# Kernel tuning notes

Measured on AMD Instinct MI355X. Metric: run time of the kernel, lower is better.

The kernel has to match this reference:

```python
import jax, jax.numpy as jnp
import numpy as np

B, L, H, NH = 8, 384, 512, 8
DH = H // NH
MAX_SEQ_LEN = 384


def setup_inputs() -> dict:
    key = jax.random.key(0)
    ks = jax.random.split(key, 16)
    s = 0.02
    seq_len = jnp.concatenate([
        jnp.array([L], dtype=jnp.int32),
        jax.random.randint(ks[3], (B - 1,), L // 2, L + 1, dtype=jnp.int32),
    ])
    return {
        "key": jax.random.normal(ks[0], (B, L, H), jnp.float32),
        "query": jax.random.normal(ks[1], (B, L, H), jnp.float32),
        "value": jax.random.normal(ks[2], (B, L, H), jnp.float32),
        "seq_len": seq_len,
        "pe": jax.random.normal(ks[4], (2 * MAX_SEQ_LEN + 1, H), jnp.float32) * s,
        "Wk": jax.random.normal(ks[5], (H, H), jnp.float32) * s,
        "bk": jnp.zeros((H,), jnp.float32),
        "Wq": jax.random.normal(ks[6], (H, H), jnp.float32) * s,
        "bq": jnp.zeros((H,), jnp.float32),
        "Wv": jax.random.normal(ks[7], (H, H), jnp.float32) * s,
        "bv": jnp.zeros((H,), jnp.float32),
        "Wr": jax.random.normal(ks[8], (H, H), jnp.float32) * s,
        "br": jnp.zeros((H,), jnp.float32),
        "u_bias": jax.random.normal(ks[9], (NH, DH), jnp.float32) * s,
        "v_bias": jax.random.normal(ks[10], (NH, DH), jnp.float32) * s,
        "Wff": jax.random.normal(ks[11], (H, H), jnp.float32) * s,
        "bff": jnp.zeros((H,), jnp.float32),
    }


def reference(key, query, value, seq_len, pe, Wk, bk, Wq, bq, Wv, bv, Wr, br, u_bias, v_bias, Wff, bff):
    # relative distances: rel[i, j] = j - i, in [-(L-1), L-1]
    rel = jnp.arange(L)[None, :] - jnp.arange(L)[:, None]          # [L, L]
    rpe = pe[rel + MAX_SEQ_LEN]                                    # [L, L, H]

    k = (key @ Wk.T + bk).reshape(B, L, NH, DH)
    q = (query @ Wq.T + bq).reshape(B, L, NH, DH)
    v = (value @ Wv.T + bv).reshape(B, L, NH, DH)
    rpe = (rpe @ Wr.T + br).reshape(L, L, NH, DH)

    # Transformer-XL score terms
    A = jnp.einsum('bihd,bjhd->bhij', q, k)                        # content-content
    Bt = jnp.einsum('bihd,ijhd->bhij', q, rpe)                     # content-position
    C = jnp.einsum('hd,bjhd->bhj', u_bias, k)[:, :, None, :]       # global content bias
    Dt = jnp.einsum('hd,ijhd->hij', v_bias, rpe)[None]             # global position bias

    scores = (A + Bt + C + Dt) / jnp.sqrt(jnp.float32(DH))
    key_mask = jnp.arange(L)[None, :] < seq_len[:, None]           # [B, L]
    scores = jnp.where(key_mask[:, None, None, :], scores, -1e15)
    attn = jax.nn.softmax(scores, axis=-1)                         # [B, NH, L, L]

    out = jnp.einsum('bhij,bjhd->bihd', attn, v).reshape(B, L, H)
    return out @ Wff.T + bff
```

## Files before the change

kernel.cpp:

```cpp
#include <hip/hip_runtime.h>
#include <hip/hip_bf16.h>

#define B_  8
#define L_  384
#define H_  512
#define NH_ 8
#define DH_ 64
#define RRM 768

typedef short bf16x8 __attribute__((ext_vector_type(8)));
typedef float f32x4  __attribute__((ext_vector_type(4)));
#define MFMA_BF16 __builtin_amdgcn_mfma_f32_16x16x32_bf16

static __device__ __forceinline__ unsigned short f2bf(float f) {
    unsigned u = __builtin_bit_cast(unsigned, f);
    u += 0x7fffu + ((u >> 16) & 1u);
    return (unsigned short)(u >> 16);
}
static __device__ __forceinline__ float bf2f(unsigned short s) {
    unsigned u = ((unsigned)s) << 16;
    return __builtin_bit_cast(float, u);
}

struct CvtArgs {
    const float* src[9];
    unsigned short* dst[9];
    int nchunks[9];
};
__global__ __launch_bounds__(256) void cvt_kernel(CvtArgs a) {
    int chunk = blockIdx.x;
    int r = 0;
    while (r < 8 && chunk >= a.nchunks[r]) { chunk -= a.nchunks[r]; r++; }
    const float4 v = ((const float4*)a.src[r])[chunk * 256 + threadIdx.x];
    ushort4 o;
    o.x = f2bf(v.x); o.y = f2bf(v.y); o.z = f2bf(v.z); o.w = f2bf(v.w);
    ((ushort4*)a.dst[r])[chunk * 256 + threadIdx.x] = o;
}

#define LDT 72

template <bool IS_FF>
__global__ __launch_bounds__(256) void gemm_nt(
    const unsigned short* __restrict__ A0, const unsigned short* __restrict__ A1,
    const unsigned short* __restrict__ A2, const unsigned short* __restrict__ A3,
    const unsigned short* __restrict__ W0, const unsigned short* __restrict__ W1,
    const unsigned short* __restrict__ W2, const unsigned short* __restrict__ W3,
    const float* __restrict__ b0, const float* __restrict__ b1,
    const float* __restrict__ b2, const float* __restrict__ b3,
    const float* __restrict__ ub, const float* __restrict__ vbias,
    unsigned short* __restrict__ qu, unsigned short* __restrict__ qv,
    unsigned short* __restrict__ kb, unsigned short* __restrict__ vT,
    unsigned short* __restrict__ rp, float* __restrict__ ff) {

    const int z = IS_FF ? 4 : blockIdx.z;
    if (!IS_FF && z == 3 && blockIdx.y >= 12) return;
    const unsigned short* A = IS_FF ? A0 : (z == 0 ? A0 : z == 1 ? A1 : z == 2 ? A2 : A3);
    const unsigned short* W = IS_FF ? W0 : (z == 0 ? W0 : z == 1 ? W1 : z == 2 ? W2 : W3);
    const float* bias       = IS_FF ? b0 : (z == 0 ? b0 : z == 1 ? b1 : z == 2 ? b2 : b3);

    __shared__ unsigned short As[2][64 * LDT];
    __shared__ unsigned short Bs[2][64 * LDT];

    const int tid = threadIdx.x;
    const int w = tid >> 6, lane = tid & 63;
    const int quad = lane >> 4, lm = lane & 15;
    const int l8r = lane >> 3, l8c = lane & 7;
    const int wr = (w & 1) * 32, wc = (w >> 1) * 32;

    const unsigned short* ag = A + (size_t)(blockIdx.y * 64 + w * 16 + l8r) * 512 + l8c * 8;
    const unsigned short* wg = W + (size_t)(blockIdx.x * 64 + w * 16 + l8r) * 512 + l8c * 8;
    const int soff = (w * 16 + l8r) * LDT + l8c * 8;

    bf16x8 pa0 = *(const bf16x8*)(ag);
    bf16x8 pa1 = *(const bf16x8*)(ag + 8 * 512);
    bf16x8 pb0 = *(const bf16x8*)(wg);
    bf16x8 pb1 = *(const bf16x8*)(wg + 8 * 512);
    *(bf16x8*)&As[0][soff]            = pa0;
    *(bf16x8*)&As[0][soff + 8 * LDT]  = pa1;
    *(bf16x8*)&Bs[0][soff]            = pb0;
    *(bf16x8*)&Bs[0][soff + 8 * LDT]  = pb1;

    f32x4 acc[2][2] = {};
    for (int kc = 0; kc < 8; ++kc) {
        __syncthreads();
        const int buf = kc & 1;
        if (kc < 7) {
            const int k0 = (kc + 1) * 64;
            pa0 = *(const bf16x8*)(ag + k0);
            pa1 = *(const bf16x8*)(ag + k0 + 8 * 512);
            pb0 = *(const bf16x8*)(wg + k0);
            pb1 = *(const bf16x8*)(wg + k0 + 8 * 512);
        }
        #pragma unroll
        for (int ks = 0; ks < 2; ++ks) {
            bf16x8 a0 = *(const bf16x8*)&As[buf][(wr + lm) * LDT + ks * 32 + quad * 8];
            bf16x8 a1 = *(const bf16x8*)&As[buf][(wr + 16 + lm) * LDT + ks * 32 + quad * 8];
            bf16x8 w0 = *(const bf16x8*)&Bs[buf][(wc + lm) * LDT + ks * 32 + quad * 8];
            bf16x8 w1 = *(const bf16x8*)&Bs[buf][(wc + 16 + lm) * LDT + ks * 32 + quad * 8];
            acc[0][0] = MFMA_BF16(a0, w0, acc[0][0], 0, 0, 0);
            acc[0][1] = MFMA_BF16(a0, w1, acc[0][1], 0, 0, 0);
            acc[1][0] = MFMA_BF16(a1, w0, acc[1][0], 0, 0, 0);
            acc[1][1] = MFMA_BF16(a1, w1, acc[1][1], 0, 0, 0);
        }
        if (kc < 7) {
            const int nb = buf ^ 1;
            *(bf16x8*)&As[nb][soff]           = pa0;
            *(bf16x8*)&As[nb][soff + 8 * LDT] = pa1;
            *(bf16x8*)&Bs[nb][soff]           = pb0;
            *(bf16x8*)&Bs[nb][soff + 8 * LDT] = pb1;
        }
    }

    #pragma unroll
    for (int si = 0; si < 2; ++si) {
        #pragma unroll
        for (int sj = 0; sj < 2; ++sj) {
            #pragma unroll
            for (int reg = 0; reg < 4; ++reg) {
                const int r = blockIdx.y * 64 + wr + si * 16 + quad * 4 + reg;
                const int c = blockIdx.x * 64 + wc + sj * 16 + lm;
                const float val = acc[si][sj][reg] + bias[c];
                if (IS_FF) {
                    ff[r * 512 + c] = val;
                } else if (z == 0) {
                    const int bb = r / L_, ii = r - bb * L_;
                    const int h = c >> 6, d = c & 63;
                    const int idx = ((bb * NH_ + h) * L_ + ii) * DH_ + d;
                    qu[idx] = f2bf((val + ub[c]) * 0.125f);
                    qv[idx] = f2bf((val + vbias[c]) * 0.125f);
                } else if (z == 1) {
                    const int bb = r / L_, ii = r - bb * L_;
                    const int h = c >> 6, d = c & 63;
                    kb[((bb * NH_ + h) * L_ + ii) * DH_ + d] = f2bf(val);
                } else if (z == 2) {
                    const int bb = r / L_, ii = r - bb * L_;
                    const int h = c >> 6, d = c & 63;
                    vT[((bb * NH_ + h) * DH_ + d) * L_ + ii] = f2bf(val);
                } else {
                    rp[r * 512 + c] = f2bf(val);
                }
            }
        }
    }
}

#define BTSTR 424
__global__ __launch_bounds__(256) void attn_fused(
    const unsigned short* __restrict__ qu, const unsigned short* __restrict__ qv,
    const unsigned short* __restrict__ kbf, const unsigned short* __restrict__ vT,
    const unsigned short* __restrict__ rp, const int* __restrict__ seq_len,
    unsigned short* __restrict__ Obf) {
    __shared__ __align__(16) unsigned short BtP[32 * BTSTR];
    __shared__ float mx_red[32][2];
    __shared__ float sm_red[32][2];
    const int lane = threadIdx.x & 63, wv = threadIdx.x >> 6;
    const int quad = lane >> 4, lm = lane & 15;
    const int bh = blockIdx.y, b = bh >> 3, h = bh & 7;
    const int i0 = blockIdx.x * 32;
    const int sl = seq_len[b];
    const int msub = wv & 1, nh = wv >> 1;
    const int m_lo = 353 - i0;
    const int i_fr = i0 + msub * 16 + lm;

    {
        const unsigned short* qvr = qv + (size_t)(bh * L_ + i_fr) * DH_;
        const bf16x8 av0 = *(const bf16x8*)(qvr + quad * 8);
        const bf16x8 av1 = *(const bf16x8*)(qvr + 32 + quad * 8);
        #pragma unroll
        for (int ns = 0; ns < 13; ++ns) {
            const int n = nh * 208 + ns * 16 + lm;
            const unsigned short* rrow = rp + (size_t)(m_lo + n) * 512 + h * 64;
            f32x4 bacc = {};
            bacc = MFMA_BF16(av0, *(const bf16x8*)(rrow + quad * 8), bacc, 0, 0, 0);
            bacc = MFMA_BF16(av1, *(const bf16x8*)(rrow + 32 + quad * 8), bacc, 0, 0, 0);
            #pragma unroll
            for (int reg = 0; reg < 4; ++reg) {
                const int il = msub * 16 + quad * 4 + reg;
                BtP[il * BTSTR + n] = f2bf(bacc[reg]);
            }
        }
    }
    const unsigned short* qur = qu + (size_t)(bh * L_ + i_fr) * DH_;
    const bf16x8 au0 = *(const bf16x8*)(qur + quad * 8);
    const bf16x8 au1 = *(const bf16x8*)(qur + 32 + quad * 8);
    __syncthreads();

    f32x4 sc[12];
    #pragma unroll
    for (int ns = 0; ns < 12; ++ns) {
        const int j = nh * 192 + ns * 16 + lm;
        const unsigned short* krow = kbf + (size_t)(bh * L_ + j) * DH_;
        f32x4 a = {};
        a = MFMA_BF16(au0, *(const bf16x8*)(krow + quad * 8), a, 0, 0, 0);
        a = MFMA_BF16(au1, *(const bf16x8*)(krow + 32 + quad * 8), a, 0, 0, 0);
        sc[ns] = a;
    }
    const int jbase = nh * 192 + lm;
    #pragma unroll
    for (int ns = 0; ns < 12; ++ns) {
        const int j = jbase + ns * 16;
        #pragma unroll
        for (int reg = 0; reg < 4; ++reg) {
            const int il = msub * 16 + quad * 4 + reg;
            float val = -1e30f;
            if (j < sl) val = sc[ns][reg] + bf2f(BtP[il * BTSTR + (j - il + 31)]);
            sc[ns][reg] = val;
        }
    }

    const int il0 = msub * 16 + quad * 4;
    float mx4[4], sm4[4], inv4[4];
    #pragma unroll
    for (int reg = 0; reg < 4; ++reg) {
        float m = sc[0][reg];
        #pragma unroll
        for (int ns = 1; ns < 12; ++ns) m = fmaxf(m, sc[ns][reg]);
        #pragma unroll
        for (int o = 1; o < 16; o <<= 1) m = fmaxf(m, __shfl_xor(m, o));
        mx4[reg] = m;
    }
    if (lm == 0) {
        #pragma unroll
        for (int reg = 0; reg < 4; ++reg) mx_red[il0 + reg][nh] = mx4[reg];
    }
    __syncthreads();
    #pragma unroll
    for (int reg = 0; reg < 4; ++reg)
        mx4[reg] = fmaxf(mx_red[il0 + reg][0], mx_red[il0 + reg][1]);
    #pragma unroll
    for (int reg = 0; reg < 4; ++reg) sm4[reg] = 0.f;
    #pragma unroll
    for (int ns = 0; ns < 12; ++ns) {
        #pragma unroll
        for (int reg = 0; reg < 4; ++reg) {
            const float e = __expf(sc[ns][reg] - mx4[reg]);
            sc[ns][reg] = e;
            sm4[reg] += e;
        }
    }
    #pragma unroll
    for (int reg = 0; reg < 4; ++reg) {
        float s = sm4[reg];
        #pragma unroll
        for (int o = 1; o < 16; o <<= 1) s += __shfl_xor(s, o);
        sm4[reg] = s;
    }
    if (lm == 0) {
        #pragma unroll
        for (int reg = 0; reg < 4; ++reg) sm_red[il0 + reg][nh] = sm4[reg];
    }
    __syncthreads();
    #pragma unroll
    for (int reg = 0; reg < 4; ++reg)
        inv4[reg] = 1.f / (sm_red[il0 + reg][0] + sm_red[il0 + reg][1]);

    #pragma unroll
    for (int ns = 0; ns < 12; ++ns) {
        const int j = jbase + ns * 16;
        #pragma unroll
        for (int reg = 0; reg < 4; ++reg)
            BtP[(il0 + reg) * BTSTR + j] = f2bf(sc[ns][reg] * inv4[reg]);
    }
    __syncthreads();

    {
        const int pr = msub * 16 + lm;
        f32x4 oacc[2] = {};
        #pragma unroll
        for (int kc = 0; kc < 12; ++kc) {
            const bf16x8 af = *(const bf16x8*)&BtP[pr * BTSTR + kc * 32 + quad * 8];
            #pragma unroll
            for (int t = 0; t < 2; ++t) {
                const int n = nh * 32 + t * 16 + lm;
                const unsigned short* vrow = vT + (size_t)(bh * DH_ + n) * L_ + kc * 32 + quad * 8;
                oacc[t] = MFMA_BF16(af, *(const bf16x8*)(vrow), oacc[t], 0, 0, 0);
            }
        }
        #pragma unroll
        for (int t = 0; t < 2; ++t) {
            #pragma unroll
            for (int reg = 0; reg < 4; ++reg) {
                const int i = i0 + msub * 16 + quad * 4 + reg;
                const int d = nh * 32 + t * 16 + lm;
                Obf[(size_t)(b * L_ + i) * H_ + h * DH_ + d] = f2bf(oacc[t][reg]);
            }
        }
    }
}

extern "C" void kernel_launch(void* const* d_in, const int* in_sizes, int n_in,
                              void* d_out, int out_size, void* d_ws, size_t ws_size,
                              hipStream_t stream) {
    const float* key    = (const float*)d_in[0];
    const float* query  = (const float*)d_in[1];
    const float* value  = (const float*)d_in[2];
    const int*   seqlen = (const int*)d_in[3];
    const float* pe     = (const float*)d_in[4];
    const float* Wk     = (const float*)d_in[5];
    const float* bk     = (const float*)d_in[6];
    const float* Wq     = (const float*)d_in[7];
    const float* bq     = (const float*)d_in[8];
    const float* Wv     = (const float*)d_in[9];
    const float* bv     = (const float*)d_in[10];
    const float* Wr     = (const float*)d_in[11];
    const float* br     = (const float*)d_in[12];
    const float* u_bias = (const float*)d_in[13];
    const float* v_bias = (const float*)d_in[14];
    const float* Wff    = (const float*)d_in[15];
    const float* bff    = (const float*)d_in[16];

    const size_t nTok  = (size_t)B_ * L_ * H_;
    const size_t nW    = (size_t)H_ * H_;
    const size_t nPe   = (size_t)RRM * H_;
    unsigned short* p  = (unsigned short*)d_ws;
    unsigned short* qbf  = p; p += nTok;
    unsigned short* kin  = p; p += nTok;
    unsigned short* vin  = p; p += nTok;
    unsigned short* pebf = p; p += nPe;
    unsigned short* Wqb  = p; p += nW;
    unsigned short* Wkb  = p; p += nW;
    unsigned short* Wvb  = p; p += nW;
    unsigned short* Wrb  = p; p += nW;
    unsigned short* Wffb = p; p += nW;
    unsigned short* qu   = p; p += nTok;
    unsigned short* qv   = p; p += nTok;
    unsigned short* kb   = p; p += nTok;
    unsigned short* vT   = p; p += nTok;
    unsigned short* rp   = p; p += nPe + 512;
    unsigned short* Obf  = qbf;

    CvtArgs ca;
    ca.src[0] = query;  ca.dst[0] = qbf;  ca.nchunks[0] = 1536;
    ca.src[1] = key;    ca.dst[1] = kin;  ca.nchunks[1] = 1536;
    ca.src[2] = value;  ca.dst[2] = vin;  ca.nchunks[2] = 1536;
    ca.src[3] = pe;     ca.dst[3] = pebf; ca.nchunks[3] = 384;
    ca.src[4] = Wq;     ca.dst[4] = Wqb;  ca.nchunks[4] = 256;
    ca.src[5] = Wk;     ca.dst[5] = Wkb;  ca.nchunks[5] = 256;
    ca.src[6] = Wv;     ca.dst[6] = Wvb;  ca.nchunks[6] = 256;
    ca.src[7] = Wr;     ca.dst[7] = Wrb;  ca.nchunks[7] = 256;
    ca.src[8] = Wff;    ca.dst[8] = Wffb; ca.nchunks[8] = 256;
    cvt_kernel<<<6272, 256, 0, stream>>>(ca);

    gemm_nt<false><<<dim3(8, 48, 4), 256, 0, stream>>>(
        qbf, kin, vin, pebf, Wqb, Wkb, Wvb, Wrb, bq, bk, bv, br,
        u_bias, v_bias, qu, qv, kb, vT, rp, nullptr);

    attn_fused<<<dim3(L_ / 32, B_ * NH_), 256, 0, stream>>>(
        qu, qv, kb, vT, rp, seqlen, Obf);

    gemm_nt<true><<<dim3(8, 48, 1), 256, 0, stream>>>(
        Obf, nullptr, nullptr, nullptr, Wffb, nullptr, nullptr, nullptr,
        bff, nullptr, nullptr, nullptr, nullptr, nullptr,
        nullptr, nullptr, nullptr, nullptr, nullptr, (float*)d_out);
}
```

Before: 161.9 us.

## Fuse fp32-to-bf16 conversion into GEMM loads and skip masked key tiles

Removes the standalone conversion kernel. The projection GEMMs now read fp32 activations and weights directly and convert them to bf16 while staging into shared memory, which saves a full read/write pass over the inputs and one kernel launch. The attention kernel also skips QK and position-score MFMA tiles, and the PV loop iterations, that lie beyond each batch's seq_len. The cost is that the GEMMs load twice the bytes per tile and convert redundantly, since weights are converted again in every block. The variable trip counts also add branch divergence.

```diff
diff --git a/kernel.cpp b/kernel.cpp
--- a/kernel.cpp
+++ b/kernel.cpp
@@ -21,32 +21,31 @@
     unsigned u = ((unsigned)s) << 16;
     return __builtin_bit_cast(float, u);
 }
-
-struct CvtArgs {
-    const float* src[9];
-    unsigned short* dst[9];
-    int nchunks[9];
-};
-__global__ __launch_bounds__(256) void cvt_kernel(CvtArgs a) {
-    int chunk = blockIdx.x;
-    int r = 0;
-    while (r < 8 && chunk >= a.nchunks[r]) { chunk -= a.nchunks[r]; r++; }
-    const float4 v = ((const float4*)a.src[r])[chunk * 256 + threadIdx.x];
-    ushort4 o;
-    o.x = f2bf(v.x); o.y = f2bf(v.y); o.z = f2bf(v.z); o.w = f2bf(v.w);
-    ((ushort4*)a.dst[r])[chunk * 256 + threadIdx.x] = o;
+static __device__ __forceinline__ unsigned pack2(float lo, float hi) {
+    return (unsigned)f2bf(lo) | ((unsigned)f2bf(hi) << 16);
+}
+static __device__ __forceinline__ void cvt_store8(unsigned short* dst, float4 a, float4 b) {
+    uint4 o;
+    o.x = pack2(a.x, a.y);
+    o.y = pack2(a.z, a.w);
+    o.z = pack2(b.x, b.y);
+    o.w = pack2(b.z, b.w);
+    *(uint4*)dst = o;
 }
 
 #define LDT 72
 
 template <bool IS_FF>
 __global__ __launch_bounds__(256) void gemm_nt(
-    const unsigned short* __restrict__ A0, const unsigned short* __restrict__ A1,
-    const unsigned short* __restrict__ A2, const unsigned short* __restrict__ A3,
-    const unsigned short* __restrict__ W0, const unsigned short* __restrict__ W1,
-    const unsigned short* __restrict__ W2, const unsigned short* __restrict__ W3,
+    const float* __restrict__ A0f, const float* __restrict__ A1f,
+    const float* __restrict__ A2f, const float* __restrict__ A3f,
+    const unsigned short* __restrict__ Abf,
+    const float* __restrict__ W0, const float* __restrict__ W1,
+    const float* __restrict__ W2, const float* __restrict__ W3,
+    const float* __restrict__ W4,
     const float* __restrict__ b0, const float* __restrict__ b1,
     const float* __restrict__ b2, const float* __restrict__ b3,
+    const float* __restrict__ b4,
     const float* __restrict__ ub, const float* __restrict__ vbias,
     unsigned short* __restrict__ qu, unsigned short* __restrict__ qv,
     unsigned short* __restrict__ kb, unsigned short* __restrict__ vT,
@@ -54,9 +53,9 @@
 
     const int z = IS_FF ? 4 : blockIdx.z;
     if (!IS_FF && z == 3 && blockIdx.y >= 12) return;
-    const unsigned short* A = IS_FF ? A0 : (z == 0 ? A0 : z == 1 ? A1 : z == 2 ? A2 : A3);
-    const unsigned short* W = IS_FF ? W0 : (z == 0 ? W0 : z == 1 ? W1 : z == 2 ? W2 : W3);
-    const float* bias       = IS_FF ? b0 : (z == 0 ? b0 : z == 1 ? b1 : z == 2 ? b2 : b3);
+    const float* Af   = IS_FF ? nullptr : (z == 0 ? A0f : z == 1 ? A1f : z == 2 ? A2f : A3f);
+    const float* W    = IS_FF ? W4 : (z == 0 ? W0 : z == 1 ? W1 : z == 2 ? W2 : W3);
+    const float* bias = IS_FF ? b4 : (z == 0 ? b0 : z == 1 ? b1 : z == 2 ? b2 : b3);
 
     __shared__ unsigned short As[2][64 * LDT];
     __shared__ unsigned short Bs[2][64 * LDT];
@@ -67,18 +66,32 @@
     const int l8r = lane >> 3, l8c = lane & 7;
     const int wr = (w & 1) * 32, wc = (w >> 1) * 32;
 
-    const unsigned short* ag = A + (size_t)(blockIdx.y * 64 + w * 16 + l8r) * 512 + l8c * 8;
-    const unsigned short* wg = W + (size_t)(blockIdx.x * 64 + w * 16 + l8r) * 512 + l8c * 8;
+    const size_t arow = (size_t)blockIdx.y * 64 + w * 16 + l8r;
+    const size_t wrow = (size_t)blockIdx.x * 64 + w * 16 + l8r;
+    const float* agf = IS_FF ? nullptr : Af + arow * 512 + l8c * 8;
+    const unsigned short* agb = IS_FF ? Abf + arow * 512 + l8c * 8 : nullptr;
+    const float* wgf = W + wrow * 512 + l8c * 8;
     const int soff = (w * 16 + l8r) * LDT + l8c * 8;
 
-    bf16x8 pa0 = *(const bf16x8*)(ag);
-    bf16x8 pa1 = *(const bf16x8*)(ag + 8 * 512);
-    bf16x8 pb0 = *(const bf16x8*)(wg);
-    bf16x8 pb1 = *(const bf16x8*)(wg + 8 * 512);
-    *(bf16x8*)&As[0][soff]            = pa0;
-    *(bf16x8*)&As[0][soff + 8 * LDT]  = pa1;
-    *(bf16x8*)&Bs[0][soff]            = pb0;
-    *(bf16x8*)&Bs[0][soff + 8 * LDT]  = pb1;
+    float4 pw0, pw1, pw2, pw3;
+    float4 pa0, pa1, pa2, pa3;
+    bf16x8 pab0, pab1;
+
+    pw0 = *(const float4*)(wgf);           pw1 = *(const float4*)(wgf + 4);
+    pw2 = *(const float4*)(wgf + 8 * 512); pw3 = *(const float4*)(wgf + 8 * 512 + 4);
+    if constexpr (!IS_FF) {
+        pa0 = *(const float4*)(agf);           pa1 = *(const float4*)(agf + 4);
+        pa2 = *(const float4*)(agf + 8 * 512); pa3 = *(const float4*)(agf + 8 * 512 + 4);
+        cvt_store8(&As[0][soff], pa0, pa1);
+        cvt_store8(&As[0][soff + 8 * LDT], pa2, pa3);
+    } else {
+        pab0 = *(const bf16x8*)(agb);
+        pab1 = *(const bf16x8*)(agb + 8 * 512);
+        *(bf16x8*)&As[0][soff] = pab0;
+        *(bf16x8*)&As[0][soff + 8 * LDT] = pab1;
+    }
+    cvt_store8(&Bs[0][soff], pw0, pw1);
+    cvt_store8(&Bs[0][soff + 8 * LDT], pw2, pw3);
 
     f32x4 acc[2][2] = {};
     for (int kc = 0; kc < 8; ++kc) {
@@ -86,10 +99,15 @@
         const int buf = kc & 1;
         if (kc < 7) {
             const int k0 = (kc + 1) * 64;
-            pa0 = *(const bf16x8*)(ag + k0);
-            pa1 = *(const bf16x8*)(ag + k0 + 8 * 512);
-            pb0 = *(const bf16x8*)(wg + k0);
-            pb1 = *(const bf16x8*)(wg + k0 + 8 * 512);
+            pw0 = *(const float4*)(wgf + k0);           pw1 = *(const float4*)(wgf + k0 + 4);
+            pw2 = *(const float4*)(wgf + k0 + 8 * 512); pw3 = *(const float4*)(wgf + k0 + 8 * 512 + 4);
+            if constexpr (!IS_FF) {
+                pa0 = *(const float4*)(agf + k0);           pa1 = *(const float4*)(agf + k0 + 4);
+                pa2 = *(const float4*)(agf + k0 + 8 * 512); pa3 = *(const float4*)(agf + k0 + 8 * 512 + 4);
+            } else {
+                pab0 = *(const bf16x8*)(agb + k0);
+                pab1 = *(const bf16x8*)(agb + k0 + 8 * 512);
+            }
         }
         #pragma unroll
         for (int ks = 0; ks < 2; ++ks) {
@@ -104,10 +122,15 @@
         }
         if (kc < 7) {
             const int nb = buf ^ 1;
-            *(bf16x8*)&As[nb][soff]           = pa0;
-            *(bf16x8*)&As[nb][soff + 8 * LDT] = pa1;
-            *(bf16x8*)&Bs[nb][soff]           = pb0;
-            *(bf16x8*)&Bs[nb][soff + 8 * LDT] = pb1;
+            if constexpr (!IS_FF) {
+                cvt_store8(&As[nb][soff], pa0, pa1);
+                cvt_store8(&As[nb][soff + 8 * LDT], pa2, pa3);
+            } else {
+                *(bf16x8*)&As[nb][soff] = pab0;
+                *(bf16x8*)&As[nb][soff + 8 * LDT] = pab1;
+            }
+            cvt_store8(&Bs[nb][soff], pw0, pw1);
+            cvt_store8(&Bs[nb][soff + 8 * LDT], pw2, pw3);
         }
     }
 
@@ -168,15 +191,18 @@
         const bf16x8 av1 = *(const bf16x8*)(qvr + 32 + quad * 8);
         #pragma unroll
         for (int ns = 0; ns < 13; ++ns) {
-            const int n = nh * 208 + ns * 16 + lm;
-            const unsigned short* rrow = rp + (size_t)(m_lo + n) * 512 + h * 64;
-            f32x4 bacc = {};
-            bacc = MFMA_BF16(av0, *(const bf16x8*)(rrow + quad * 8), bacc, 0, 0, 0);
-            bacc = MFMA_BF16(av1, *(const bf16x8*)(rrow + 32 + quad * 8), bacc, 0, 0, 0);
-            #pragma unroll
-            for (int reg = 0; reg < 4; ++reg) {
-                const int il = msub * 16 + quad * 4 + reg;
-                BtP[il * BTSTR + n] = f2bf(bacc[reg]);
+            const int ntl = nh * 208 + ns * 16;
+            if (ntl <= sl + 30) {
+                const int n = ntl + lm;
+                const unsigned short* rrow = rp + (size_t)(m_lo + n) * 512 + h * 64;
+                f32x4 bacc = {};
+                bacc = MFMA_BF16(av0, *(const bf16x8*)(rrow + quad * 8), bacc, 0, 0, 0);
+                bacc = MFMA_BF16(av1, *(const bf16x8*)(rrow + 32 + quad * 8), bacc, 0, 0, 0);
+                #pragma unroll
+                for (int reg = 0; reg < 4; ++reg) {
+                    const int il = msub * 16 + quad * 4 + reg;
+                    BtP[il * BTSTR + n] = f2bf(bacc[reg]);
+                }
             }
         }
     }
@@ -188,12 +214,16 @@
     f32x4 sc[12];
     #pragma unroll
     for (int ns = 0; ns < 12; ++ns) {
-        const int j = nh * 192 + ns * 16 + lm;
-        const unsigned short* krow = kbf + (size_t)(bh * L_ + j) * DH_;
-        f32x4 a = {};
-        a = MFMA_BF16(au0, *(const bf16x8*)(krow + quad * 8), a, 0, 0, 0);
-        a = MFMA_BF16(au1, *(const bf16x8*)(krow + 32 + quad * 8), a, 0, 0, 0);
-        sc[ns] = a;
+        const int jt = nh * 192 + ns * 16;
+        if (jt < sl) {
+            const unsigned short* krow = kbf + (size_t)(bh * L_ + jt + lm) * DH_;
+            f32x4 a = {};
+            a = MFMA_BF16(au0, *(const bf16x8*)(krow + quad * 8), a, 0, 0, 0);
+            a = MFMA_BF16(au1, *(const bf16x8*)(krow + 32 + quad * 8), a, 0, 0, 0);
+            sc[ns] = a;
+        } else {
+            sc[ns] = f32x4{-1e30f, -1e30f, -1e30f, -1e30f};
+        }
     }
     const int jbase = nh * 192 + lm;
     #pragma unroll
@@ -265,9 +295,9 @@
 
     {
         const int pr = msub * 16 + lm;
+        const int nkc = (sl + 31) >> 5;
         f32x4 oacc[2] = {};
-        #pragma unroll
-        for (int kc = 0; kc < 12; ++kc) {
+        for (int kc = 0; kc < nkc; ++kc) {
             const bf16x8 af = *(const bf16x8*)&BtP[pr * BTSTR + kc * 32 + quad * 8];
             #pragma unroll
             for (int t = 0; t < 2; ++t) {
@@ -309,47 +339,34 @@
     const float* Wff    = (const float*)d_in[15];
     const float* bff    = (const float*)d_in[16];
 
-    const size_t nTok  = (size_t)B_ * L_ * H_;
-    const size_t nW    = (size_t)H_ * H_;
-    const size_t nPe   = (size_t)RRM * H_;
+    const size_t nTok = (size_t)B_ * L_ * H_;
+    const size_t nPe  = (size_t)RRM * H_;
     unsigned short* p  = (unsigned short*)d_ws;
-    unsigned short* qbf  = p; p += nTok;
-    unsigned short* kin  = p; p += nTok;
-    unsigned short* vin  = p; p += nTok;
-    unsigned short* pebf = p; p += nPe;
-    unsigned short* Wqb  = p; p += nW;
-    unsigned short* Wkb  = p; p += nW;
-    unsigned short* Wvb  = p; p += nW;
-    unsigned short* Wrb  = p; p += nW;
-    unsigned short* Wffb = p; p += nW;
-    unsigned short* qu   = p; p += nTok;
-    unsigned short* qv   = p; p += nTok;
-    unsigned short* kb   = p; p += nTok;
-    unsigned short* vT   = p; p += nTok;
-    unsigned short* rp   = p; p += nPe + 512;
-    unsigned short* Obf  = qbf;
-
-    CvtArgs ca;
-    ca.src[0] = query;  ca.dst[0] = qbf;  ca.nchunks[0] = 1536;
-    ca.src[1] = key;    ca.dst[1] = kin;  ca.nchunks[1] = 1536;
-    ca.src[2] = value;  ca.dst[2] = vin;  ca.nchunks[2] = 1536;
-    ca.src[3] = pe;     ca.dst[3] = pebf; ca.nchunks[3] = 384;
-    ca.src[4] = Wq;     ca.dst[4] = Wqb;  ca.nchunks[4] = 256;
-    ca.src[5] = Wk;     ca.dst[5] = Wkb;  ca.nchunks[5] = 256;
-    ca.src[6] = Wv;     ca.dst[6] = Wvb;  ca.nchunks[6] = 256;
-    ca.src[7] = Wr;     ca.dst[7] = Wrb;  ca.nchunks[7] = 256;
-    ca.src[8] = Wff;    ca.dst[8] = Wffb; ca.nchunks[8] = 256;
-    cvt_kernel<<<6272, 256, 0, stream>>>(ca);
+    unsigned short* qu  = p; p += nTok;
+    unsigned short* qv  = p; p += nTok;
+    unsigned short* kb  = p; p += nTok;
+    unsigned short* vT  = p; p += nTok;
+    unsigned short* rp  = p; p += nPe + 512;
+    unsigned short* Obf = p; p += nTok;
 
     gemm_nt<false><<<dim3(8, 48, 4), 256, 0, stream>>>(
-        qbf, kin, vin, pebf, Wqb, Wkb, Wvb, Wrb, bq, bk, bv, br,
-        u_bias, v_bias, qu, qv, kb, vT, rp, nullptr);
+         query, key, value, pe,
+         nullptr,
+         Wq, Wk, Wv, Wr, nullptr,
+         bq, bk, bv, br, nullptr,
+         u_bias, v_bias,
+         qu, qv, kb, vT, rp,
+         nullptr);
 
     attn_fused<<<dim3(L_ / 32, B_ * NH_), 256, 0, stream>>>(
         qu, qv, kb, vT, rp, seqlen, Obf);
 
     gemm_nt<true><<<dim3(8, 48, 1), 256, 0, stream>>>(
-        Obf, nullptr, nullptr, nullptr, Wffb, nullptr, nullptr, nullptr,
-        bff, nullptr, nullptr, nullptr, nullptr, nullptr,
-        nullptr, nullptr, nullptr, nullptr, nullptr, (float*)d_out);
-}
+         nullptr, nullptr, nullptr, nullptr,
+         Obf,
+         nullptr, nullptr, nullptr, nullptr, Wff,
+         nullptr, nullptr, nullptr, nullptr, bff,
+         nullptr, nullptr,
+         nullptr, nullptr, nullptr, nullptr, nullptr,
+         (float*)d_out);
+}
```

After: 161.5 us. No clear change (-0.2%).

## Use direct global-to-LDS loads with XOR swizzle and skip masked attention tiles

Applied to the files above, without the earlier changes.

The GEMM staging now uses global_load_lds to write tiles straight into LDS with an XOR-swizzled unpadded layout, instead of going through registers with a padded stride. The attention kernel skips QK and position-bias MFMA tiles beyond the key sequence length and shortens the PV loop to the valid key range. This cuts register traffic and wasted work on masked keys. The risk is ordering: the async LDS loads are only covered by __syncthreads, with no explicit wait on the loads.

```diff
diff --git a/kernel.cpp b/kernel.cpp
--- a/kernel.cpp
+++ b/kernel.cpp
@@ -20,6 +20,13 @@
 static __device__ __forceinline__ float bf2f(unsigned short s) {
     unsigned u = ((unsigned)s) << 16;
     return __builtin_bit_cast(float, u);
+}
+
+typedef unsigned int u32;
+static __device__ __forceinline__ void glds16(const void* g, void* l) {
+    __builtin_amdgcn_global_load_lds(
+        (const __attribute__((address_space(1))) u32*)g,
+        (__attribute__((address_space(3))) u32*)l, 16, 0, 0);
 }
 
 struct CvtArgs {
@@ -37,16 +44,17 @@
     ((ushort4*)a.dst[r])[chunk * 256 + threadIdx.x] = o;
 }
 
-#define LDT 72
-
 template <bool IS_FF>
 __global__ __launch_bounds__(256) void gemm_nt(
     const unsigned short* __restrict__ A0, const unsigned short* __restrict__ A1,
     const unsigned short* __restrict__ A2, const unsigned short* __restrict__ A3,
+    const unsigned short* __restrict__ A4,
     const unsigned short* __restrict__ W0, const unsigned short* __restrict__ W1,
     const unsigned short* __restrict__ W2, const unsigned short* __restrict__ W3,
+    const unsigned short* __restrict__ W4,
     const float* __restrict__ b0, const float* __restrict__ b1,
     const float* __restrict__ b2, const float* __restrict__ b3,
+    const float* __restrict__ b4,
     const float* __restrict__ ub, const float* __restrict__ vbias,
     unsigned short* __restrict__ qu, unsigned short* __restrict__ qv,
     unsigned short* __restrict__ kb, unsigned short* __restrict__ vT,
@@ -54,72 +62,62 @@
 
     const int z = IS_FF ? 4 : blockIdx.z;
     if (!IS_FF && z == 3 && blockIdx.y >= 12) return;
-    const unsigned short* A = IS_FF ? A0 : (z == 0 ? A0 : z == 1 ? A1 : z == 2 ? A2 : A3);
-    const unsigned short* W = IS_FF ? W0 : (z == 0 ? W0 : z == 1 ? W1 : z == 2 ? W2 : W3);
-    const float* bias       = IS_FF ? b0 : (z == 0 ? b0 : z == 1 ? b1 : z == 2 ? b2 : b3);
-
-    __shared__ unsigned short As[2][64 * LDT];
-    __shared__ unsigned short Bs[2][64 * LDT];
+    const unsigned short* A = z == 0 ? A0 : z == 1 ? A1 : z == 2 ? A2 : z == 3 ? A3 : A4;
+    const unsigned short* W = z == 0 ? W0 : z == 1 ? W1 : z == 2 ? W2 : z == 3 ? W3 : W4;
+    const float* bias       = z == 0 ? b0 : z == 1 ? b1 : z == 2 ? b2 : z == 3 ? b3 : b4;
+
+    __shared__ unsigned short AsF[2 * 64 * 64];
+    __shared__ unsigned short BsF[2 * 64 * 64];
 
     const int tid = threadIdx.x;
     const int w = tid >> 6, lane = tid & 63;
     const int quad = lane >> 4, lm = lane & 15;
-    const int l8r = lane >> 3, l8c = lane & 7;
     const int wr = (w & 1) * 32, wc = (w >> 1) * 32;
 
-    const unsigned short* ag = A + (size_t)(blockIdx.y * 64 + w * 16 + l8r) * 512 + l8c * 8;
-    const unsigned short* wg = W + (size_t)(blockIdx.x * 64 + w * 16 + l8r) * 512 + l8c * 8;
-    const int soff = (w * 16 + l8r) * LDT + l8c * 8;
-
-    bf16x8 pa0 = *(const bf16x8*)(ag);
-    bf16x8 pa1 = *(const bf16x8*)(ag + 8 * 512);
-    bf16x8 pb0 = *(const bf16x8*)(wg);
-    bf16x8 pb1 = *(const bf16x8*)(wg + 8 * 512);
-    *(bf16x8*)&As[0][soff]            = pa0;
-    *(bf16x8*)&As[0][soff + 8 * LDT]  = pa1;
-    *(bf16x8*)&Bs[0][soff]            = pb0;
-    *(bf16x8*)&Bs[0][soff + 8 * LDT]  = pb1;
+    const int sr = lane >> 3, sj = lane & 7;
+    const unsigned short* ga = A + (size_t)(blockIdx.y * 64 + w * 16 + sr) * 512 + (sj ^ sr) * 8;
+    const unsigned short* gb = W + (size_t)(blockIdx.x * 64 + w * 16 + sr) * 512 + (sj ^ sr) * 8;
+
+    auto stage = [&](int kc, int buf) {
+        #pragma unroll
+        for (int t = 0; t < 2; ++t) {
+            int off = buf * 4096 + (w * 16 + t * 8) * 64;
+            off = __builtin_amdgcn_readfirstlane(off);
+            glds16(ga + kc * 64 + t * 8 * 512, &AsF[off]);
+            glds16(gb + kc * 64 + t * 8 * 512, &BsF[off]);
+        }
+    };
 
     f32x4 acc[2][2] = {};
+    stage(0, 0);
     for (int kc = 0; kc < 8; ++kc) {
         __syncthreads();
         const int buf = kc & 1;
-        if (kc < 7) {
-            const int k0 = (kc + 1) * 64;
-            pa0 = *(const bf16x8*)(ag + k0);
-            pa1 = *(const bf16x8*)(ag + k0 + 8 * 512);
-            pb0 = *(const bf16x8*)(wg + k0);
-            pb1 = *(const bf16x8*)(wg + k0 + 8 * 512);
-        }
+        if (kc < 7) stage(kc + 1, buf ^ 1);
+        const int base = buf * 4096;
         #pragma unroll
         for (int ks = 0; ks < 2; ++ks) {
-            bf16x8 a0 = *(const bf16x8*)&As[buf][(wr + lm) * LDT + ks * 32 + quad * 8];
-            bf16x8 a1 = *(const bf16x8*)&As[buf][(wr + 16 + lm) * LDT + ks * 32 + quad * 8];
-            bf16x8 w0 = *(const bf16x8*)&Bs[buf][(wc + lm) * LDT + ks * 32 + quad * 8];
-            bf16x8 w1 = *(const bf16x8*)&Bs[buf][(wc + 16 + lm) * LDT + ks * 32 + quad * 8];
+            const int s = (((ks * 4 + quad) ^ (lm & 7))) * 8;
+            bf16x8 a0 = *(const bf16x8*)&AsF[base + (wr + lm) * 64 + s];
+            bf16x8 a1 = *(const bf16x8*)&AsF[base + (wr + 16 + lm) * 64 + s];
+            bf16x8 w0 = *(const bf16x8*)&BsF[base + (wc + lm) * 64 + s];
+            bf16x8 w1 = *(const bf16x8*)&BsF[base + (wc + 16 + lm) * 64 + s];
             acc[0][0] = MFMA_BF16(a0, w0, acc[0][0], 0, 0, 0);
             acc[0][1] = MFMA_BF16(a0, w1, acc[0][1], 0, 0, 0);
             acc[1][0] = MFMA_BF16(a1, w0, acc[1][0], 0, 0, 0);
             acc[1][1] = MFMA_BF16(a1, w1, acc[1][1], 0, 0, 0);
         }
-        if (kc < 7) {
-            const int nb = buf ^ 1;
-            *(bf16x8*)&As[nb][soff]           = pa0;
-            *(bf16x8*)&As[nb][soff + 8 * LDT] = pa1;
-            *(bf16x8*)&Bs[nb][soff]           = pb0;
-            *(bf16x8*)&Bs[nb][soff + 8 * LDT] = pb1;
-        }
     }
 
     #pragma unroll
     for (int si = 0; si < 2; ++si) {
         #pragma unroll
-        for (int sj = 0; sj < 2; ++sj) {
+        for (int sj2 = 0; sj2 < 2; ++sj2) {
             #pragma unroll
             for (int reg = 0; reg < 4; ++reg) {
                 const int r = blockIdx.y * 64 + wr + si * 16 + quad * 4 + reg;
-                const int c = blockIdx.x * 64 + wc + sj * 16 + lm;
-                const float val = acc[si][sj][reg] + bias[c];
+                const int c = blockIdx.x * 64 + wc + sj2 * 16 + lm;
+                const float val = acc[si][sj2][reg] + bias[c];
                 if (IS_FF) {
                     ff[r * 512 + c] = val;
                 } else if (z == 0) {
@@ -168,15 +166,18 @@
         const bf16x8 av1 = *(const bf16x8*)(qvr + 32 + quad * 8);
         #pragma unroll
         for (int ns = 0; ns < 13; ++ns) {
-            const int n = nh * 208 + ns * 16 + lm;
-            const unsigned short* rrow = rp + (size_t)(m_lo + n) * 512 + h * 64;
-            f32x4 bacc = {};
-            bacc = MFMA_BF16(av0, *(const bf16x8*)(rrow + quad * 8), bacc, 0, 0, 0);
-            bacc = MFMA_BF16(av1, *(const bf16x8*)(rrow + 32 + quad * 8), bacc, 0, 0, 0);
-            #pragma unroll
-            for (int reg = 0; reg < 4; ++reg) {
-                const int il = msub * 16 + quad * 4 + reg;
-                BtP[il * BTSTR + n] = f2bf(bacc[reg]);
+            const int ntl = nh * 208 + ns * 16;
+            if (ntl <= sl + 30) {
+                const int n = ntl + lm;
+                const unsigned short* rrow = rp + (size_t)(m_lo + n) * 512 + h * 64;
+                f32x4 bacc = {};
+                bacc = MFMA_BF16(av0, *(const bf16x8*)(rrow + quad * 8), bacc, 0, 0, 0);
+                bacc = MFMA_BF16(av1, *(const bf16x8*)(rrow + 32 + quad * 8), bacc, 0, 0, 0);
+                #pragma unroll
+                for (int reg = 0; reg < 4; ++reg) {
+                    const int il = msub * 16 + quad * 4 + reg;
+                    BtP[il * BTSTR + n] = f2bf(bacc[reg]);
+                }
             }
         }
     }
@@ -188,12 +189,16 @@
     f32x4 sc[12];
     #pragma unroll
     for (int ns = 0; ns < 12; ++ns) {
-        const int j = nh * 192 + ns * 16 + lm;
-        const unsigned short* krow = kbf + (size_t)(bh * L_ + j) * DH_;
-        f32x4 a = {};
-        a = MFMA_BF16(au0, *(const bf16x8*)(krow + quad * 8), a, 0, 0, 0);
-        a = MFMA_BF16(au1, *(const bf16x8*)(krow + 32 + quad * 8), a, 0, 0, 0);
-        sc[ns] = a;
+        const int jt = nh * 192 + ns * 16;
+        if (jt < sl) {
+            const unsigned short* krow = kbf + (size_t)(bh * L_ + jt + lm) * DH_;
+            f32x4 a = {};
+            a = MFMA_BF16(au0, *(const bf16x8*)(krow + quad * 8), a, 0, 0, 0);
+            a = MFMA_BF16(au1, *(const bf16x8*)(krow + 32 + quad * 8), a, 0, 0, 0);
+            sc[ns] = a;
+        } else {
+            sc[ns] = f32x4{-1e30f, -1e30f, -1e30f, -1e30f};
+        }
     }
     const int jbase = nh * 192 + lm;
     #pragma unroll
@@ -265,9 +270,9 @@
 
     {
         const int pr = msub * 16 + lm;
+        const int nkc = (sl + 31) >> 5;
         f32x4 oacc[2] = {};
-        #pragma unroll
-        for (int kc = 0; kc < 12; ++kc) {
+        for (int kc = 0; kc < nkc; ++kc) {
             const bf16x8 af = *(const bf16x8*)&BtP[pr * BTSTR + kc * 32 + quad * 8];
             #pragma unroll
             for (int t = 0; t < 2; ++t) {
@@ -309,9 +314,9 @@
     const float* Wff    = (const float*)d_in[15];
     const float* bff    = (const float*)d_in[16];
 
-    const size_t nTok  = (size_t)B_ * L_ * H_;
-    const size_t nW    = (size_t)H_ * H_;
-    const size_t nPe   = (size_t)RRM * H_;
+    const size_t nTok = (size_t)B_ * L_ * H_;
+    const size_t nPe  = (size_t)RRM * H_;
+    const size_t nW   = (size_t)H_ * H_;
     unsigned short* p  = (unsigned short*)d_ws;
     unsigned short* qbf  = p; p += nTok;
     unsigned short* kin  = p; p += nTok;
@@ -342,14 +347,21 @@
     cvt_kernel<<<6272, 256, 0, stream>>>(ca);
 
     gemm_nt<false><<<dim3(8, 48, 4), 256, 0, stream>>>(
-        qbf, kin, vin, pebf, Wqb, Wkb, Wvb, Wrb, bq, bk, bv, br,
-        u_bias, v_bias, qu, qv, kb, vT, rp, nullptr);
+         qbf, kin, vin, pebf, nullptr,
+         Wqb, Wkb, Wvb, Wrb, nullptr,
+         bq, bk, bv, br, nullptr,
+         u_bias, v_bias,
+         qu, qv, kb, vT, rp,
+         nullptr);
 
     attn_fused<<<dim3(L_ / 32, B_ * NH_), 256, 0, stream>>>(
         qu, qv, kb, vT, rp, seqlen, Obf);
 
     gemm_nt<true><<<dim3(8, 48, 1), 256, 0, stream>>>(
-        Obf, nullptr, nullptr, nullptr, Wffb, nullptr, nullptr, nullptr,
-        bff, nullptr, nullptr, nullptr, nullptr, nullptr,
-        nullptr, nullptr, nullptr, nullptr, nullptr, (float*)d_out);
-}
+         nullptr, nullptr, nullptr, nullptr, Obf,
+         nullptr, nullptr, nullptr, nullptr, Wffb,
+         nullptr, nullptr, nullptr, nullptr, bff,
+         nullptr, nullptr,
+         nullptr, nullptr, nullptr, nullptr, nullptr,
+         (float*)d_out);
+}
```

New measurement: 161.0 us. About the same (-0.6%).
